# Performance work log

Measured on AMD Instinct MI355X. Metric: run time of the kernel, lower is better.

Reference implementation:

```python
import jax, jax.numpy as jnp
import numpy as np

M, K, N, G = 64, 4096, 11008, 128  # tokens, infeatures, outfeatures, group_size
NUM_GROUPS = K // G  # 32


def _fp8_round_trip(w):
    # Simulate FP8 E4M3 storage of the quantized weight codes.
    return w.astype(jnp.float8_e4m3fn).astype(jnp.float32)


def setup_inputs() -> dict:
    key = jax.random.key(0)
    k1, k2, k3, k4 = jax.random.split(key, 4)
    x = jax.random.normal(k1, (M, K), dtype=jnp.float32)
    # FP8-representable weight codes (post round-trip, stored as f32 values)
    weight = _fp8_round_trip(jax.random.normal(k2, (N, K), dtype=jnp.float32) * 2.0)
    # Per-(out_feature, group) dequant scales, strictly positive
    weight_scale = jax.random.uniform(k3, (N, NUM_GROUPS), dtype=jnp.float32,
                                      minval=0.005, maxval=0.02)
    bias = jax.random.normal(k4, (N,), dtype=jnp.float32)
    return {"x": x, "weight": weight, "weight_scale": weight_scale, "bias": bias}


def reference(x, weight, weight_scale, bias):
    # Dequantize: each group of `G` consecutive in-features of an output row
    # shares one scale -> w_deq[o, i] = weight[o, i] * scale[o, i // G]
    n, k = weight.shape
    g = k // weight_scale.shape[1]
    w_deq = (weight.reshape(n, -1, g) * weight_scale[:, :, None]).reshape(n, k)
    # Fused dequant-matmul: out[m, o] = sum_i x[m, i] * w_deq[o, i] + bias[o]
    out = jnp.einsum("mk,nk->mn", x, w_deq) + bias
    return out
```

## Files before the change

### kernel.cpp

```cpp
#include <hip/hip_runtime.h>


#define Md 64
#define Kd 4096
#define Nd 11008
#define NGROUPS 32
#define BN 64
#define KSPLIT 16
#define KCHUNK 256
#define NSTEP 8
#define WS_PART_BYTES ((size_t)KSPLIT * Md * Nd * 4)

typedef __attribute__((ext_vector_type(8))) __bf16 bf16x8;
typedef __attribute__((ext_vector_type(4))) float f32x4;

__global__ __launch_bounds__(256)
void xcvt_kernel(const float* __restrict__ x, __bf16* __restrict__ xbf)
{
    const int tid = blockIdx.x * 256 + threadIdx.x;
    const int m   = tid >> 9;
    const int kgg = tid & 511;
    const float* xp = x + (size_t)m * Kd + kgg * 8;
    float4 a = *(const float4*)xp;
    float4 b = *(const float4*)(xp + 4);
    bf16x8 v = {(__bf16)a.x, (__bf16)a.y, (__bf16)a.z, (__bf16)a.w,
                (__bf16)b.x, (__bf16)b.y, (__bf16)b.z, (__bf16)b.w};
    *(bf16x8*)(xbf + ((size_t)kgg * 64 + m) * 8) = v;
}

__global__ __launch_bounds__(256, 4)
void qlinear_pass1(const __bf16* __restrict__ xbf,
                   const float* __restrict__ w,
                   const float* __restrict__ scale,
                   float* __restrict__ ws)
{
    const int tid  = threadIdx.x;
    const int wv   = tid >> 6;
    const int lane = tid & 63;
    const int quad = lane >> 4;
    const int ln   = lane & 15;

    const int n0 = blockIdx.x * BN;
    const int ky = blockIdx.y;

    const int nrow = n0 + wv * 16 + ln;
    const float* wp = w + (size_t)nrow * Kd + ky * KCHUNK + quad * 8;

    const float2 sc2 = *(const float2*)(scale + (size_t)nrow * NGROUPS + ky * 2);
    const float sc[2] = {sc2.x, sc2.y};

    const __bf16* xb = xbf + ((size_t)ky * 32 * 64) * 8
                     + ((size_t)quad * 64 + ln) * 8;

    bf16x8 xq[2][4];
    #pragma unroll
    for (int t = 0; t < 4; ++t)
        xq[0][t] = *(const bf16x8*)(xb + (size_t)t * 16 * 8);

    float4 wreg[16];
    #pragma unroll
    for (int s = 0; s < NSTEP; ++s) {
        wreg[2 * s]     = *(const float4*)(wp + s * 32);
        wreg[2 * s + 1] = *(const float4*)(wp + s * 32 + 4);
    }

    f32x4 acc[4];
    #pragma unroll
    for (int t = 0; t < 4; ++t) acc[t] = (f32x4){0.f, 0.f, 0.f, 0.f};

    #pragma unroll
    for (int s = 0; s < NSTEP; ++s) {
        if (s + 1 < NSTEP) {
            const __bf16* xn = xb + (size_t)(s + 1) * 4 * 64 * 8;
            #pragma unroll
            for (int t = 0; t < 4; ++t)
                xq[(s + 1) & 1][t] = *(const bf16x8*)(xn + (size_t)t * 16 * 8);
        }

        const float ss = sc[s >> 2];
        const float4 wa = wreg[2 * s], wb = wreg[2 * s + 1];
        bf16x8 wf = {(__bf16)(wa.x * ss), (__bf16)(wa.y * ss),
                     (__bf16)(wa.z * ss), (__bf16)(wa.w * ss),
                     (__bf16)(wb.x * ss), (__bf16)(wb.y * ss),
                     (__bf16)(wb.z * ss), (__bf16)(wb.w * ss)};

        #pragma unroll
        for (int t = 0; t < 4; ++t)
            acc[t] = __builtin_amdgcn_mfma_f32_16x16x32_bf16(xq[s & 1][t], wf,
                                                             acc[t], 0, 0, 0);
    }

    float* op = ws + ((size_t)ky * Md) * Nd + n0 + wv * 16 + ln;
    #pragma unroll
    for (int t = 0; t < 4; ++t)
        #pragma unroll
        for (int r = 0; r < 4; ++r)
            op[(size_t)(t * 16 + quad * 4 + r) * Nd] = acc[t][r];
}

__global__ __launch_bounds__(256)
void qlinear_reduce(const float* __restrict__ ws,
                    const float* __restrict__ bias,
                    float* __restrict__ out)
{
    const int idx4 = blockIdx.x * 256 + threadIdx.x;
    if (idx4 >= Md * Nd / 4) return;
    const int n4 = idx4 % (Nd / 4);
    float4 v = *(const float4*)(bias + n4 * 4);
    #pragma unroll
    for (int ky = 0; ky < KSPLIT; ++ky) {
        float4 p = *(const float4*)(ws + (size_t)ky * Md * Nd + (size_t)idx4 * 4);
        v.x += p.x; v.y += p.y; v.z += p.z; v.w += p.w;
    }
    *(float4*)(out + (size_t)idx4 * 4) = v;
}

extern "C" void kernel_launch(void* const* d_in, const int* in_sizes, int n_in,
                              void* d_out, int out_size, void* d_ws, size_t ws_size,
                              hipStream_t stream) {
    const float* x     = (const float*)d_in[0];
    const float* w     = (const float*)d_in[1];
    const float* scale = (const float*)d_in[2];
    const float* bias  = (const float*)d_in[3];
    float* out = (float*)d_out;

    float*  ws_part = (float*)d_ws;
    __bf16* xbf     = (__bf16*)((char*)d_ws + WS_PART_BYTES);

    xcvt_kernel<<<128, 256, 0, stream>>>(x, xbf);

    dim3 grid1(Nd / BN, KSPLIT);
    qlinear_pass1<<<grid1, 256, 0, stream>>>(xbf, w, scale, ws_part);

    const int total4 = Md * Nd / 4;
    qlinear_reduce<<<(total4 + 255) / 256, 256, 0, stream>>>(ws_part, bias, out);
}
```

Measured before the change: 287.8 us.

## Halve K-split, stream weight loads with rolling prefetch, store partials in MFMA layout

```diff
diff --git a/kernel.cpp b/kernel.cpp
--- a/kernel.cpp
+++ b/kernel.cpp
@@ -6,9 +6,10 @@
 #define Nd 11008
 #define NGROUPS 32
 #define BN 64
-#define KSPLIT 16
-#define KCHUNK 256
-#define NSTEP 8
+#define KSPLIT 8
+#define KCHUNK 512
+#define NSTEP 16
+#define NGRP 4
 #define WS_PART_BYTES ((size_t)KSPLIT * Md * Nd * 4)
 
 typedef __attribute__((ext_vector_type(8))) __bf16 bf16x8;
@@ -46,22 +47,22 @@
     const int nrow = n0 + wv * 16 + ln;
     const float* wp = w + (size_t)nrow * Kd + ky * KCHUNK + quad * 8;
 
-    const float2 sc2 = *(const float2*)(scale + (size_t)nrow * NGROUPS + ky * 2);
-    const float sc[2] = {sc2.x, sc2.y};
+    float4 sc4 = *(const float4*)(scale + (size_t)nrow * NGROUPS + ky * NGRP);
+    const float sc[4] = {sc4.x, sc4.y, sc4.z, sc4.w};
 
-    const __bf16* xb = xbf + ((size_t)ky * 32 * 64) * 8
-                     + ((size_t)quad * 64 + ln) * 8;
+    const __bf16* xb = xbf + (((size_t)ky * 64 + quad) * 64 + ln) * 8;
 
-    bf16x8 xq[2][4];
+    bf16x8 xq[3][4];
+    float4 wb[4][2];
     #pragma unroll
-    for (int t = 0; t < 4; ++t)
-        xq[0][t] = *(const bf16x8*)(xb + (size_t)t * 16 * 8);
-
-    float4 wreg[16];
+    for (int s = 0; s < 2; ++s)
+        #pragma unroll
+        for (int t = 0; t < 4; ++t)
+            xq[s][t] = *(const bf16x8*)(xb + (size_t)(s * 256 + t * 16) * 8);
     #pragma unroll
-    for (int s = 0; s < NSTEP; ++s) {
-        wreg[2 * s]     = *(const float4*)(wp + s * 32);
-        wreg[2 * s + 1] = *(const float4*)(wp + s * 32 + 4);
+    for (int s = 0; s < 3; ++s) {
+        wb[s][0] = *(const float4*)(wp + s * 32);
+        wb[s][1] = *(const float4*)(wp + s * 32 + 4);
     }
 
     f32x4 acc[4];
@@ -70,32 +71,35 @@
 
     #pragma unroll
     for (int s = 0; s < NSTEP; ++s) {
-        if (s + 1 < NSTEP) {
-            const __bf16* xn = xb + (size_t)(s + 1) * 4 * 64 * 8;
+        if (s + 3 < NSTEP) {
+            wb[(s + 3) & 3][0] = *(const float4*)(wp + (s + 3) * 32);
+            wb[(s + 3) & 3][1] = *(const float4*)(wp + (s + 3) * 32 + 4);
+        }
+        if (s + 2 < NSTEP) {
+            const __bf16* xn = xb + (size_t)((s + 2) * 256) * 8;
             #pragma unroll
             for (int t = 0; t < 4; ++t)
-                xq[(s + 1) & 1][t] = *(const bf16x8*)(xn + (size_t)t * 16 * 8);
+                xq[(s + 2) % 3][t] = *(const bf16x8*)(xn + (size_t)(t * 16) * 8);
         }
 
         const float ss = sc[s >> 2];
-        const float4 wa = wreg[2 * s], wb = wreg[2 * s + 1];
+        const float4 wa = wb[s & 3][0], wc = wb[s & 3][1];
         bf16x8 wf = {(__bf16)(wa.x * ss), (__bf16)(wa.y * ss),
                      (__bf16)(wa.z * ss), (__bf16)(wa.w * ss),
-                     (__bf16)(wb.x * ss), (__bf16)(wb.y * ss),
-                     (__bf16)(wb.z * ss), (__bf16)(wb.w * ss)};
+                     (__bf16)(wc.x * ss), (__bf16)(wc.y * ss),
+                     (__bf16)(wc.z * ss), (__bf16)(wc.w * ss)};
 
         #pragma unroll
         for (int t = 0; t < 4; ++t)
-            acc[t] = __builtin_amdgcn_mfma_f32_16x16x32_bf16(xq[s & 1][t], wf,
+            acc[t] = __builtin_amdgcn_mfma_f32_16x16x32_bf16(xq[s % 3][t], wf,
                                                              acc[t], 0, 0, 0);
     }
 
-    float* op = ws + ((size_t)ky * Md) * Nd + n0 + wv * 16 + ln;
+    float* op = ws + (size_t)ky * (Md * Nd)
+              + ((size_t)blockIdx.x * 4 + wv) * 1024 + lane * 4;
     #pragma unroll
     for (int t = 0; t < 4; ++t)
-        #pragma unroll
-        for (int r = 0; r < 4; ++r)
-            op[(size_t)(t * 16 + quad * 4 + r) * Nd] = acc[t][r];
+        *(f32x4*)(op + t * 256) = acc[t];
 }
 
 __global__ __launch_bounds__(256)
@@ -105,14 +109,27 @@
 {
     const int idx4 = blockIdx.x * 256 + threadIdx.x;
     if (idx4 >= Md * Nd / 4) return;
-    const int n4 = idx4 % (Nd / 4);
-    float4 v = *(const float4*)(bias + n4 * 4);
+
+    const int lane = idx4 & 63;
+    const int t    = (idx4 >> 6) & 3;
+    const int bw   = idx4 >> 8;
+    const int quad = lane >> 4;
+    const int ln   = lane & 15;
+    const int n    = (bw >> 2) * 64 + (bw & 3) * 16 + ln;
+    const int m0   = t * 16 + quad * 4;
+
+    float4 v = {0.f, 0.f, 0.f, 0.f};
     #pragma unroll
     for (int ky = 0; ky < KSPLIT; ++ky) {
-        float4 p = *(const float4*)(ws + (size_t)ky * Md * Nd + (size_t)idx4 * 4);
+        float4 p = *(const float4*)(ws + (size_t)ky * (Md * Nd)
+                                    + (size_t)idx4 * 4);
         v.x += p.x; v.y += p.y; v.z += p.z; v.w += p.w;
     }
-    *(float4*)(out + (size_t)idx4 * 4) = v;
+    const float b = bias[n];
+    out[(size_t)(m0 + 0) * Nd + n] = v.x + b;
+    out[(size_t)(m0 + 1) * Nd + n] = v.y + b;
+    out[(size_t)(m0 + 2) * Nd + n] = v.z + b;
+    out[(size_t)(m0 + 3) * Nd + n] = v.w + b;
 }
 
 extern "C" void kernel_launch(void* const* d_in, const int* in_sizes, int n_in,
```

Result: faster. 279.5 us (-2.9%).
